# Kernel optimization log

Measured on AMD Instinct MI355X. Metric: run time of the kernel, lower is better.

## Reference

```python
import jax, jax.numpy as jnp
import numpy as np

N_NODES = 100000
N_EDGES = 1600000
NODE_DIM = 128
EDGE_DIM = 32
HIDDEN_DIM = 256


def _linear_params(key, fan_in, fan_out):
    kw, kb = jax.random.split(key)
    bound = 1.0 / np.sqrt(fan_in)
    W = jax.random.uniform(kw, (fan_in, fan_out), minval=-bound, maxval=bound, dtype=jnp.float32)
    b = jax.random.uniform(kb, (fan_out,), minval=-bound, maxval=bound, dtype=jnp.float32)
    return W, b


def setup_inputs() -> dict:
    key = jax.random.key(0)
    ks = jax.random.split(key, 8)
    x = jax.random.normal(ks[0], (N_NODES, NODE_DIM), dtype=jnp.float32)
    edge_index = jax.random.randint(ks[1], (2, N_EDGES), 0, N_NODES, dtype=jnp.int64)
    edge_attr = jax.random.normal(ks[2], (N_EDGES, EDGE_DIM), dtype=jnp.float32)
    congestion = jax.random.uniform(ks[3], (N_NODES,), dtype=jnp.float32)
    msg_in = 2 * NODE_DIM + EDGE_DIM + 1
    mW1, mb1 = _linear_params(ks[4], msg_in, HIDDEN_DIM)
    mW2, mb2 = _linear_params(ks[5], HIDDEN_DIM, NODE_DIM)
    uW1, ub1 = _linear_params(ks[6], 2 * NODE_DIM, HIDDEN_DIM)
    uW2, ub2 = _linear_params(ks[7], HIDDEN_DIM, NODE_DIM)
    return {
        "x": x, "edge_index": edge_index, "edge_attr": edge_attr, "congestion": congestion,
        "mW1": mW1, "mb1": mb1, "mW2": mW2, "mb2": mb2,
        "uW1": uW1, "ub1": ub1, "uW2": uW2, "ub2": ub2,
    }


def reference(x, edge_index, edge_attr, congestion, mW1, mb1, mW2, mb2, uW1, ub1, uW2, ub2):
    src, dst = edge_index[0], edge_index[1]
    # gather node features and src congestion, concat along feature dim  [E, 2D+edge_dim+1]
    msg_in = jnp.concatenate(
        [x[src], x[dst], edge_attr, congestion[src][:, None]], axis=-1)
    h = jax.nn.relu(msg_in @ mW1 + mb1)          # [E, hidden]
    messages = h @ mW2 + mb2                     # [E, node_dim]
    # scatter_add messages into destination nodes  [N, node_dim]
    aggregated = jax.ops.segment_sum(messages, dst, num_segments=x.shape[0])
    upd_in = jnp.concatenate([x, aggregated], axis=-1)  # [N, 2*node_dim]
    h2 = jax.nn.relu(upd_in @ uW1 + ub1)
    x_new = h2 @ uW2 + ub2                       # [N, node_dim]
    return x_new
```

## Files before the change

### kernel.cpp

```cpp
#include <hip/hip_runtime.h>

#define E_TOTAL 1600000
#define NN 100000
#define D 128
#define ED 32
#define H 256

typedef __attribute__((ext_vector_type(8))) short s16x8;
typedef __attribute__((ext_vector_type(4))) short s16x4;
typedef __attribute__((ext_vector_type(4))) float f32x4;

#define MFMA(a, b, c) __builtin_amdgcn_mfma_f32_16x16x32_bf16((a), (b), (c), 0, 0, 0)

__device__ __forceinline__ short f2bf(float f) {
    unsigned u = __builtin_bit_cast(unsigned, f);
    u += 0x7fffu + ((u >> 16) & 1u);
    return (short)(u >> 16);
}

__device__ __forceinline__ void gll16(const void* g, void* l) {
    __builtin_amdgcn_global_load_lds(
        (const __attribute__((address_space(1))) void*)g,
        (__attribute__((address_space(3))) void*)l, 16, 0, 0);
}

__global__ void k_cvt_x(const float* __restrict__ x, short* __restrict__ xb, int n) {
    int i = (blockIdx.x * blockDim.x + threadIdx.x) * 4;
    if (i >= n) return;
    f32x4 v = *(const f32x4*)(x + i);
    s16x4 o;
    o[0] = f2bf(v[0]); o[1] = f2bf(v[1]); o[2] = f2bf(v[2]); o[3] = f2bf(v[3]);
    *(s16x4*)(xb + i) = o;
}

__global__ void k_swz(const float* __restrict__ W, short* __restrict__ out,
                      int K, int N, int total) {
    int idx = blockIdx.x * blockDim.x + threadIdx.x;
    if (idx >= total) return;
    int j    = idx & 7;
    int lane = (idx >> 3) & 63;
    int rest = idx >> 9;
    int NT   = N >> 4;
    int nt   = rest % NT;
    int t    = rest / NT;
    int k    = t * 32 + (lane >> 4) * 8 + j;
    int col  = nt * 16 + (lane & 15);
    float v  = (k < K) ? W[k * N + col] : 0.f;
    out[idx] = f2bf(v);
}

__global__ void k_hist(const int* __restrict__ ei, int* __restrict__ cnt) {
    int e = blockIdx.x * blockDim.x + threadIdx.x;
    if (e >= E_TOTAL) return;
    atomicAdd(&cnt[ei[E_TOTAL + e]], 1);
}

__global__ void k_scan1(int* __restrict__ cnt, int* __restrict__ psum, int n) {
    __shared__ int wsum[16];
    __shared__ int woff[16];
    const int tid = threadIdx.x, lane = tid & 63, wv = tid >> 6;
    int i = blockIdx.x * 1024 + tid;
    int v = (i < n) ? cnt[i] : 0;
    int s = v;
#pragma unroll
    for (int off = 1; off < 64; off <<= 1) {
        int u = __shfl_up(s, off, 64);
        if (lane >= off) s += u;
    }
    if (lane == 63) wsum[wv] = s;
    __syncthreads();
    if (wv == 0 && lane < 16) {
        int t = wsum[lane];
        int sc = t;
#pragma unroll
        for (int off = 1; off < 16; off <<= 1) {
            int u = __shfl_up(sc, off, 16);
            if (lane >= off) sc += u;
        }
        woff[lane] = sc - t;
    }
    __syncthreads();
    int excl = (s - v) + woff[wv];
    if (i < n) cnt[i] = excl;
    if (tid == 1023) psum[blockIdx.x] = excl + v;
}

__global__ void k_scan2(int* __restrict__ psum, int nb) {
    __shared__ int w0;
    const int tid = threadIdx.x, lane = tid & 63, wv = tid >> 6;
    int v = (tid < nb) ? psum[tid] : 0;
    int s = v;
#pragma unroll
    for (int off = 1; off < 64; off <<= 1) {
        int u = __shfl_up(s, off, 64);
        if (lane >= off) s += u;
    }
    if (wv == 0 && lane == 63) w0 = s;
    __syncthreads();
    int excl = (s - v) + (wv ? w0 : 0);
    if (tid < nb) psum[tid] = excl;
}

__global__ void k_scan3(const int* __restrict__ psum, int* __restrict__ cnt, int n) {
    int i = blockIdx.x * 1024 + threadIdx.x;
    if (i < n) cnt[i] += psum[blockIdx.x];
}

__global__ void k_perm(const int* __restrict__ ei, int* __restrict__ cursor,
                       int* __restrict__ perm, int2* __restrict__ srcdst) {
    int e = blockIdx.x * blockDim.x + threadIdx.x;
    if (e >= E_TOTAL) return;
    int s = ei[e], d = ei[E_TOTAL + e];
    int pos = atomicAdd(&cursor[d], 1);
    perm[pos] = e;
    srcdst[pos] = make_int2(s, d);
}

__global__ __launch_bounds__(256, 2)
void k_edge(const short* __restrict__ xb, const int* __restrict__ perm,
            const int2* __restrict__ srcdst,
            const float* __restrict__ eattr, const float* __restrict__ cong,
            const short* __restrict__ W1s, const float* __restrict__ b1,
            const short* __restrict__ W2s, const float* __restrict__ b2,
            float* __restrict__ agg) {
    __shared__ char smem[73728];
    __shared__ int   dst_s[128];
    __shared__ short cong_s[128];

    const int tid  = threadIdx.x;
    const int lane = tid & 63;
    const int w    = tid >> 6;
    const int m    = lane & 15;
    const int q    = lane >> 4;
    const int p0b  = blockIdx.x * 128;

    {
        const int kqs = (lane & 3) ^ ((lane >> 4) & 3);
#pragma unroll
        for (int j = 0; j < 2; j++) {
            int el  = w * 32 + j * 16 + (lane >> 2);
            int2 sd = srcdst[p0b + el];
            int  ea = perm[p0b + el];
            char* dst = smem + (w * 2 + j) * 1024;
            const char* gx0 = (const char*)xb + (long)sd.x * 256 + kqs * 16;
            const char* gx1 = (const char*)xb + (long)sd.y * 256 + kqs * 16;
#pragma unroll
            for (int t = 0; t < 4; t++)
                gll16(gx0 + t * 64, dst + t * 8192);
#pragma unroll
            for (int t = 0; t < 4; t++)
                gll16(gx1 + t * 64, dst + (4 + t) * 8192);
            const float* ge = eattr + (long)ea * ED + kqs * 8;
            f32x4 e0 = *(const f32x4*)ge, e1 = *(const f32x4*)(ge + 4);
            s16x8 ev;
#pragma unroll
            for (int jj = 0; jj < 4; jj++) { ev[jj] = f2bf(e0[jj]); ev[4 + jj] = f2bf(e1[jj]); }
            *(s16x8*)(dst + 8 * 8192 + lane * 16) = ev;
        }
        if (tid < 128) {
            int2 sd2 = srcdst[p0b + tid];
            dst_s[tid]  = sd2.y;
            cong_s[tid] = f2bf(cong[sd2.x]);
        }
    }
    __syncthreads();

    const int rdoff = m * 64 + ((q ^ ((m >> 2) & 3)) << 4);

    f32x4 acc[8][4];
#pragma unroll
    for (int mt = 0; mt < 8; mt++)
#pragma unroll
        for (int n = 0; n < 4; n++) acc[mt][n] = (f32x4){0.f, 0.f, 0.f, 0.f};

#pragma unroll
    for (int t = 0; t < 9; t++) {
        s16x8 b[4];
        const short* bw = W1s + (t * 16 + w * 4) * 512 + lane * 8;
#pragma unroll
        for (int n = 0; n < 4; n++) b[n] = *(const s16x8*)(bw + n * 512);
#pragma unroll
        for (int mt = 0; mt < 8; mt++) {
            s16x8 a = *(const s16x8*)(smem + t * 8192 + mt * 1024 + rdoff);
#pragma unroll
            for (int n = 0; n < 4; n++) acc[mt][n] = MFMA(a, b[n], acc[mt][n]);
        }
    }
    {
        s16x8 b[4];
        const short* bw = W1s + (9 * 16 + w * 4) * 512 + lane * 8;
#pragma unroll
        for (int n = 0; n < 4; n++) b[n] = *(const s16x8*)(bw + n * 512);
#pragma unroll
        for (int mt = 0; mt < 8; mt++) {
            s16x8 a = (s16x8){0, 0, 0, 0, 0, 0, 0, 0};
            short cv = cong_s[mt * 16 + m];
            a[0] = (q == 0) ? cv : (short)0;
#pragma unroll
            for (int n = 0; n < 4; n++) acc[mt][n] = MFMA(a, b[n], acc[mt][n]);
        }
    }
    __syncthreads();

    {
        short* hb = (short*)smem;
#pragma unroll
        for (int n = 0; n < 4; n++) {
            const int chunk = 2 * w + (n >> 1);
            const int srq   = (n & 1) * 2 + (m >> 3);
            const int phys  = srq ^ q;
            const float bias = b1[w * 64 + n * 16 + m];
            const int base = chunk * 4096 + (q * 4) * 32 + phys * 8 + (m & 7);
#pragma unroll
            for (int mt = 0; mt < 8; mt++) {
#pragma unroll
                for (int r = 0; r < 4; r++) {
                    float v = acc[mt][n][r] + bias;
                    hb[base + mt * 512 + r * 32] = f2bf(v > 0.f ? v : 0.f);
                }
            }
        }
    }
    __syncthreads();

    f32x4 acc2[8][2];
#pragma unroll
    for (int mt = 0; mt < 8; mt++) {
        acc2[mt][0] = (f32x4){0.f, 0.f, 0.f, 0.f};
        acc2[mt][1] = (f32x4){0.f, 0.f, 0.f, 0.f};
    }
#pragma unroll
    for (int t2 = 0; t2 < 8; t2++) {
        s16x8 b0  = *(const s16x8*)(W2s + (t2 * 8 + w * 2) * 512 + lane * 8);
        s16x8 b1v = *(const s16x8*)(W2s + (t2 * 8 + w * 2 + 1) * 512 + lane * 8);
#pragma unroll
        for (int mt = 0; mt < 8; mt++) {
            s16x8 a = *(const s16x8*)(smem + t2 * 8192 + mt * 1024 + rdoff);
            acc2[mt][0] = MFMA(a, b0, acc2[mt][0]);
            acc2[mt][1] = MFMA(a, b1v, acc2[mt][1]);
        }
    }
    __syncthreads();

    {
        float (*mbuf)[132] = (float (*)[132])smem;
        float bb0 = b2[w * 32 + m];
        float bb1 = b2[w * 32 + 16 + m];
#pragma unroll
        for (int mt = 0; mt < 8; mt++)
#pragma unroll
            for (int r = 0; r < 4; r++) {
                mbuf[mt * 16 + q * 4 + r][w * 32 + m]      = acc2[mt][0][r] + bb0;
                mbuf[mt * 16 + q * 4 + r][w * 32 + 16 + m] = acc2[mt][1][r] + bb1;
            }
    }
    __syncthreads();

    {
        float (*mbuf)[132] = (float (*)[132])smem;
        const int half = tid >> 7, cc = tid & 127;
        float s = 0.f;
        int prev = dst_s[half * 64];
        for (int row = half * 64; row < half * 64 + 64; row++) {
            int dcur = dst_s[row];
            if (dcur != prev) {
                __hip_atomic_fetch_add(agg + (long)prev * D + cc, s,
                                       __ATOMIC_RELAXED, __HIP_MEMORY_SCOPE_AGENT);
                s = 0.f; prev = dcur;
            }
            s += mbuf[row][cc];
        }
        __hip_atomic_fetch_add(agg + (long)prev * D + cc, s,
                               __ATOMIC_RELAXED, __HIP_MEMORY_SCOPE_AGENT);
    }
}

__global__ __launch_bounds__(256, 2)
void k_node(const short* __restrict__ xb, const float* __restrict__ agg,
            const short* __restrict__ U1s, const float* __restrict__ b1,
            const short* __restrict__ U2s, const float* __restrict__ b2,
            float* __restrict__ out) {
    __shared__ char smem[65536];
    const int tid  = threadIdx.x;
    const int lane = tid & 63;
    const int w    = tid >> 6;
    const int m    = lane & 15;
    const int q    = lane >> 4;
    const int r0   = blockIdx.x * 128;

    {
        const int kqs = (lane & 3) ^ ((lane >> 4) & 3);
#pragma unroll
        for (int j = 0; j < 2; j++) {
            int rowl = w * 32 + j * 16 + (lane >> 2);
            int grow = r0 + rowl;
            int gc   = grow < NN ? grow : 0;
            char* dst = smem + (w * 2 + j) * 1024;
            const char* gx = (const char*)xb + (long)gc * 256 + kqs * 16;
#pragma unroll
            for (int t = 0; t < 4; t++)
                gll16(gx + t * 64, dst + t * 8192);
            const float* ga = agg + (long)gc * D + kqs * 8;
#pragma unroll
            for (int t = 0; t < 4; t++) {
                f32x4 a0 = *(const f32x4*)(ga + t * 32);
                f32x4 a1 = *(const f32x4*)(ga + t * 32 + 4);
                s16x8 v;
#pragma unroll
                for (int jj = 0; jj < 4; jj++) { v[jj] = f2bf(a0[jj]); v[4 + jj] = f2bf(a1[jj]); }
                *(s16x8*)(dst + (4 + t) * 8192 + lane * 16) = v;
            }
        }
    }
    __syncthreads();

    const int rdoff = m * 64 + ((q ^ ((m >> 2) & 3)) << 4);

    f32x4 acc[8][4];
#pragma unroll
    for (int mt = 0; mt < 8; mt++)
#pragma unroll
        for (int n = 0; n < 4; n++) acc[mt][n] = (f32x4){0.f, 0.f, 0.f, 0.f};

#pragma unroll
    for (int t = 0; t < 8; t++) {
        s16x8 b[4];
        const short* bw = U1s + (t * 16 + w * 4) * 512 + lane * 8;
#pragma unroll
        for (int n = 0; n < 4; n++) b[n] = *(const s16x8*)(bw + n * 512);
#pragma unroll
        for (int mt = 0; mt < 8; mt++) {
            s16x8 a = *(const s16x8*)(smem + t * 8192 + mt * 1024 + rdoff);
#pragma unroll
            for (int n = 0; n < 4; n++) acc[mt][n] = MFMA(a, b[n], acc[mt][n]);
        }
    }
    __syncthreads();

    {
        short* hb = (short*)smem;
#pragma unroll
        for (int n = 0; n < 4; n++) {
            const int chunk = 2 * w + (n >> 1);
            const int srq   = (n & 1) * 2 + (m >> 3);
            const int phys  = srq ^ q;
            const float bias = b1[w * 64 + n * 16 + m];
            const int base = chunk * 4096 + (q * 4) * 32 + phys * 8 + (m & 7);
#pragma unroll
            for (int mt = 0; mt < 8; mt++) {
#pragma unroll
                for (int r = 0; r < 4; r++) {
                    float v = acc[mt][n][r] + bias;
                    hb[base + mt * 512 + r * 32] = f2bf(v > 0.f ? v : 0.f);
                }
            }
        }
    }
    __syncthreads();

    f32x4 acc2[8][2];
#pragma unroll
    for (int mt = 0; mt < 8; mt++) {
        acc2[mt][0] = (f32x4){0.f, 0.f, 0.f, 0.f};
        acc2[mt][1] = (f32x4){0.f, 0.f, 0.f, 0.f};
    }
#pragma unroll
    for (int t2 = 0; t2 < 8; t2++) {
        s16x8 b0  = *(const s16x8*)(U2s + (t2 * 8 + w * 2) * 512 + lane * 8);
        s16x8 b1v = *(const s16x8*)(U2s + (t2 * 8 + w * 2 + 1) * 512 + lane * 8);
#pragma unroll
        for (int mt = 0; mt < 8; mt++) {
            s16x8 a = *(const s16x8*)(smem + t2 * 8192 + mt * 1024 + rdoff);
            acc2[mt][0] = MFMA(a, b0, acc2[mt][0]);
            acc2[mt][1] = MFMA(a, b1v, acc2[mt][1]);
        }
    }

    {
        float bb0 = b2[w * 32 + m];
        float bb1 = b2[w * 32 + 16 + m];
#pragma unroll
        for (int mt = 0; mt < 8; mt++)
#pragma unroll
            for (int r = 0; r < 4; r++) {
                int grow = r0 + mt * 16 + q * 4 + r;
                if (grow < NN) {
                    out[(long)grow * D + w * 32 + m]      = acc2[mt][0][r] + bb0;
                    out[(long)grow * D + w * 32 + 16 + m] = acc2[mt][1][r] + bb1;
                }
            }
    }
}

extern "C" void kernel_launch(void* const* d_in, const int* in_sizes, int n_in,
                              void* d_out, int out_size, void* d_ws, size_t ws_size,
                              hipStream_t stream) {
    const float* x     = (const float*)d_in[0];
    const int*   ei    = (const int*)d_in[1];
    const float* eattr = (const float*)d_in[2];
    const float* cong  = (const float*)d_in[3];
    const float* mW1   = (const float*)d_in[4];
    const float* mb1   = (const float*)d_in[5];
    const float* mW2   = (const float*)d_in[6];
    const float* mb2   = (const float*)d_in[7];
    const float* uW1   = (const float*)d_in[8];
    const float* ub1   = (const float*)d_in[9];
    const float* uW2   = (const float*)d_in[10];
    const float* ub2   = (const float*)d_in[11];

    char* ws = (char*)d_ws;
    float* agg    = (float*)ws;
    short* xb     = (short*)(ws + 51200000);
    short* W1s    = (short*)(ws + 76800000);
    short* W2s    = (short*)(ws + 76963840);
    short* U1s    = (short*)(ws + 77029376);
    short* U2s    = (short*)(ws + 77160448);
    int*   cnt    = (int*)(ws + 77225984);
    int*   perm   = (int*)(ws + 77625984);
    int2*  srcdst = (int2*)(ws + 84025984);
    int*   psum   = (int*)(ws + 96825984);

    hipMemsetAsync(agg, 0, (size_t)NN * D * sizeof(float), stream);
    hipMemsetAsync(cnt, 0, (size_t)NN * sizeof(int), stream);

    k_cvt_x<<<(NN * D / 4 + 255) / 256, 256, 0, stream>>>(x, xb, NN * D);

    int tW1 = 10 * 16 * 512, tW2 = 8 * 8 * 512, tU1 = 8 * 16 * 512, tU2 = 8 * 8 * 512;
    k_swz<<<(tW1 + 255) / 256, 256, 0, stream>>>(mW1, W1s, 289, 256, tW1);
    k_swz<<<(tW2 + 255) / 256, 256, 0, stream>>>(mW2, W2s, 256, 128, tW2);
    k_swz<<<(tU1 + 255) / 256, 256, 0, stream>>>(uW1, U1s, 256, 256, tU1);
    k_swz<<<(tU2 + 255) / 256, 256, 0, stream>>>(uW2, U2s, 256, 128, tU2);

    int nb = (NN + 1023) / 1024;
    k_hist<<<(E_TOTAL + 255) / 256, 256, 0, stream>>>(ei, cnt);
    k_scan1<<<nb, 1024, 0, stream>>>(cnt, psum, NN);
    k_scan2<<<1, 128, 0, stream>>>(psum, nb);
    k_scan3<<<nb, 1024, 0, stream>>>(psum, cnt, NN);
    k_perm<<<(E_TOTAL + 255) / 256, 256, 0, stream>>>(ei, cnt, perm, srcdst);

    k_edge<<<E_TOTAL / 128, 256, 0, stream>>>(xb, perm, srcdst, eattr, cong,
                                              W1s, mb1, W2s, mb2, agg);
    k_node<<<(NN + 127) / 128, 256, 0, stream>>>(xb, agg, U1s, ub1, U2s, ub2,
                                                 (float*)d_out);
}
```

Before: 1.055 ms.

## Split edge and node MLP tiles across eight waves to double occupancy

Both k_edge and k_node move from 256 to 512 threads per block. The eight waves are arranged as two row halves by four column groups, so each wave now holds a 4x4 accumulator tile instead of 8x4. The LDS staging layout and swizzle keys are reworked to match the new row ownership, and the segmented atomic reduction now runs over four 32-row quarters. The aim is to cut per-wave register pressure and fit more waves per CU to hide gather latency. In exchange, each weight fragment is loaded twice per block and the edge kernel may issue slightly more atomics.

```diff
diff --git a/kernel.cpp b/kernel.cpp
--- a/kernel.cpp
+++ b/kernel.cpp
@@ -116,7 +116,7 @@
     srcdst[pos] = make_int2(s, d);
 }
 
-__global__ __launch_bounds__(256, 2)
+__global__ __launch_bounds__(512, 4)
 void k_edge(const short* __restrict__ xb, const int* __restrict__ perm,
             const int2* __restrict__ srcdst,
             const float* __restrict__ eattr, const float* __restrict__ cong,
@@ -130,33 +130,31 @@
     const int tid  = threadIdx.x;
     const int lane = tid & 63;
     const int w    = tid >> 6;
+    const int eh   = w >> 2;
+    const int cg   = w & 3;
     const int m    = lane & 15;
     const int q    = lane >> 4;
     const int p0b  = blockIdx.x * 128;
 
     {
-        const int kqs = (lane & 3) ^ ((lane >> 4) & 3);
-#pragma unroll
-        for (int j = 0; j < 2; j++) {
-            int el  = w * 32 + j * 16 + (lane >> 2);
-            int2 sd = srcdst[p0b + el];
-            int  ea = perm[p0b + el];
-            char* dst = smem + (w * 2 + j) * 1024;
-            const char* gx0 = (const char*)xb + (long)sd.x * 256 + kqs * 16;
-            const char* gx1 = (const char*)xb + (long)sd.y * 256 + kqs * 16;
-#pragma unroll
-            for (int t = 0; t < 4; t++)
-                gll16(gx0 + t * 64, dst + t * 8192);
-#pragma unroll
-            for (int t = 0; t < 4; t++)
-                gll16(gx1 + t * 64, dst + (4 + t) * 8192);
-            const float* ge = eattr + (long)ea * ED + kqs * 8;
-            f32x4 e0 = *(const f32x4*)ge, e1 = *(const f32x4*)(ge + 4);
-            s16x8 ev;
-#pragma unroll
-            for (int jj = 0; jj < 4; jj++) { ev[jj] = f2bf(e0[jj]); ev[4 + jj] = f2bf(e1[jj]); }
-            *(s16x8*)(dst + 8 * 8192 + lane * 16) = ev;
-        }
+        int edge = w * 16 + (lane >> 2);
+        int2 sd  = srcdst[p0b + edge];
+        int kqs  = (lane & 3) ^ ((lane >> 3) & 3);
+        const char* gx0 = (const char*)xb + (long)sd.x * 256 + kqs * 16;
+        const char* gx1 = (const char*)xb + (long)sd.y * 256 + kqs * 16;
+#pragma unroll
+        for (int t = 0; t < 4; t++)
+            gll16(gx0 + t * 64, smem + t * 8192 + w * 1024);
+#pragma unroll
+        for (int t = 0; t < 4; t++)
+            gll16(gx1 + t * 64, smem + (4 + t) * 8192 + w * 1024);
+        int ea = perm[p0b + edge];
+        const float* ge = eattr + (long)ea * ED + kqs * 8;
+        f32x4 e0 = *(const f32x4*)ge, e1 = *(const f32x4*)(ge + 4);
+        s16x8 ev;
+#pragma unroll
+        for (int j = 0; j < 4; j++) { ev[j] = f2bf(e0[j]); ev[4 + j] = f2bf(e1[j]); }
+        *(s16x8*)(smem + 8 * 8192 + w * 1024 + lane * 16) = ev;
         if (tid < 128) {
             int2 sd2 = srcdst[p0b + tid];
             dst_s[tid]  = sd2.y;
@@ -165,36 +163,36 @@
     }
     __syncthreads();
 
-    const int rdoff = m * 64 + ((q ^ ((m >> 2) & 3)) << 4);
-
-    f32x4 acc[8][4];
-#pragma unroll
-    for (int mt = 0; mt < 8; mt++)
+    const int rdoff = m * 64 + ((q ^ ((m >> 1) & 3)) << 4);
+
+    f32x4 acc[4][4];
+#pragma unroll
+    for (int mt = 0; mt < 4; mt++)
 #pragma unroll
         for (int n = 0; n < 4; n++) acc[mt][n] = (f32x4){0.f, 0.f, 0.f, 0.f};
 
 #pragma unroll
     for (int t = 0; t < 9; t++) {
         s16x8 b[4];
-        const short* bw = W1s + (t * 16 + w * 4) * 512 + lane * 8;
+        const short* bw = W1s + (t * 16 + cg * 4) * 512 + lane * 8;
 #pragma unroll
         for (int n = 0; n < 4; n++) b[n] = *(const s16x8*)(bw + n * 512);
 #pragma unroll
-        for (int mt = 0; mt < 8; mt++) {
-            s16x8 a = *(const s16x8*)(smem + t * 8192 + mt * 1024 + rdoff);
+        for (int mt = 0; mt < 4; mt++) {
+            s16x8 a = *(const s16x8*)(smem + t * 8192 + (eh * 4 + mt) * 1024 + rdoff);
 #pragma unroll
             for (int n = 0; n < 4; n++) acc[mt][n] = MFMA(a, b[n], acc[mt][n]);
         }
     }
     {
         s16x8 b[4];
-        const short* bw = W1s + (9 * 16 + w * 4) * 512 + lane * 8;
+        const short* bw = W1s + (9 * 16 + cg * 4) * 512 + lane * 8;
 #pragma unroll
         for (int n = 0; n < 4; n++) b[n] = *(const s16x8*)(bw + n * 512);
 #pragma unroll
-        for (int mt = 0; mt < 8; mt++) {
+        for (int mt = 0; mt < 4; mt++) {
             s16x8 a = (s16x8){0, 0, 0, 0, 0, 0, 0, 0};
-            short cv = cong_s[mt * 16 + m];
+            short cv = cong_s[eh * 64 + mt * 16 + m];
             a[0] = (q == 0) ? cv : (short)0;
 #pragma unroll
             for (int n = 0; n < 4; n++) acc[mt][n] = MFMA(a, b[n], acc[mt][n]);
@@ -203,39 +201,42 @@
     __syncthreads();
 
     {
-        short* hb = (short*)smem;
+        short* hb16 = (short*)smem;
 #pragma unroll
         for (int n = 0; n < 4; n++) {
-            const int chunk = 2 * w + (n >> 1);
+            const int chunk = 2 * cg + (n >> 1);
             const int srq   = (n & 1) * 2 + (m >> 3);
-            const int phys  = srq ^ q;
-            const float bias = b1[w * 64 + n * 16 + m];
-            const int base = chunk * 4096 + (q * 4) * 32 + phys * 8 + (m & 7);
-#pragma unroll
-            for (int mt = 0; mt < 8; mt++) {
+            const float bias = b1[cg * 64 + n * 16 + m];
+#pragma unroll
+            for (int mt = 0; mt < 4; mt++) {
 #pragma unroll
                 for (int r = 0; r < 4; r++) {
-                    float v = acc[mt][n][r] + bias;
-                    hb[base + mt * 512 + r * 32] = f2bf(v > 0.f ? v : 0.f);
+                    int edge = eh * 64 + mt * 16 + q * 4 + r;
+                    int key  = (2 * q + (r >> 1)) & 3;
+                    int phys = srq ^ key;
+                    float v  = acc[mt][n][r] + bias;
+                    hb16[chunk * 4096 + edge * 32 + phys * 8 + (m & 7)] =
+                        f2bf(v > 0.f ? v : 0.f);
                 }
             }
         }
     }
     __syncthreads();
 
-    f32x4 acc2[8][2];
-#pragma unroll
-    for (int mt = 0; mt < 8; mt++) {
+    f32x4 acc2[4][2];
+#pragma unroll
+    for (int mt = 0; mt < 4; mt++) {
         acc2[mt][0] = (f32x4){0.f, 0.f, 0.f, 0.f};
         acc2[mt][1] = (f32x4){0.f, 0.f, 0.f, 0.f};
     }
 #pragma unroll
     for (int t2 = 0; t2 < 8; t2++) {
-        s16x8 b0  = *(const s16x8*)(W2s + (t2 * 8 + w * 2) * 512 + lane * 8);
-        s16x8 b1v = *(const s16x8*)(W2s + (t2 * 8 + w * 2 + 1) * 512 + lane * 8);
-#pragma unroll
-        for (int mt = 0; mt < 8; mt++) {
-            s16x8 a = *(const s16x8*)(smem + t2 * 8192 + mt * 1024 + rdoff);
+        const short* bw = W2s + (t2 * 8 + cg * 2) * 512 + lane * 8;
+        s16x8 b0  = *(const s16x8*)bw;
+        s16x8 b1v = *(const s16x8*)(bw + 512);
+#pragma unroll
+        for (int mt = 0; mt < 4; mt++) {
+            s16x8 a = *(const s16x8*)(smem + t2 * 8192 + (eh * 4 + mt) * 1024 + rdoff);
             acc2[mt][0] = MFMA(a, b0, acc2[mt][0]);
             acc2[mt][1] = MFMA(a, b1v, acc2[mt][1]);
         }
@@ -244,24 +245,25 @@
 
     {
         float (*mbuf)[132] = (float (*)[132])smem;
-        float bb0 = b2[w * 32 + m];
-        float bb1 = b2[w * 32 + 16 + m];
-#pragma unroll
-        for (int mt = 0; mt < 8; mt++)
+        float bb0 = b2[cg * 32 + m];
+        float bb1 = b2[cg * 32 + 16 + m];
+#pragma unroll
+        for (int mt = 0; mt < 4; mt++)
 #pragma unroll
             for (int r = 0; r < 4; r++) {
-                mbuf[mt * 16 + q * 4 + r][w * 32 + m]      = acc2[mt][0][r] + bb0;
-                mbuf[mt * 16 + q * 4 + r][w * 32 + 16 + m] = acc2[mt][1][r] + bb1;
+                int edge = eh * 64 + mt * 16 + q * 4 + r;
+                mbuf[edge][cg * 32 + m]      = acc2[mt][0][r] + bb0;
+                mbuf[edge][cg * 32 + 16 + m] = acc2[mt][1][r] + bb1;
             }
     }
     __syncthreads();
 
     {
         float (*mbuf)[132] = (float (*)[132])smem;
-        const int half = tid >> 7, cc = tid & 127;
+        const int qtr = tid >> 7, cc = tid & 127;
         float s = 0.f;
-        int prev = dst_s[half * 64];
-        for (int row = half * 64; row < half * 64 + 64; row++) {
+        int prev = dst_s[qtr * 32];
+        for (int row = qtr * 32; row < qtr * 32 + 32; row++) {
             int dcur = dst_s[row];
             if (dcur != prev) {
                 __hip_atomic_fetch_add(agg + (long)prev * D + cc, s,
@@ -275,7 +277,7 @@
     }
 }
 
-__global__ __launch_bounds__(256, 2)
+__global__ __launch_bounds__(512, 4)
 void k_node(const short* __restrict__ xb, const float* __restrict__ agg,
             const short* __restrict__ U1s, const float* __restrict__ b1,
             const short* __restrict__ U2s, const float* __restrict__ b2,
@@ -284,53 +286,51 @@
     const int tid  = threadIdx.x;
     const int lane = tid & 63;
     const int w    = tid >> 6;
+    const int eh   = w >> 2;
+    const int cg   = w & 3;
     const int m    = lane & 15;
     const int q    = lane >> 4;
     const int r0   = blockIdx.x * 128;
 
     {
-        const int kqs = (lane & 3) ^ ((lane >> 4) & 3);
-#pragma unroll
-        for (int j = 0; j < 2; j++) {
-            int rowl = w * 32 + j * 16 + (lane >> 2);
-            int grow = r0 + rowl;
-            int gc   = grow < NN ? grow : 0;
-            char* dst = smem + (w * 2 + j) * 1024;
-            const char* gx = (const char*)xb + (long)gc * 256 + kqs * 16;
-#pragma unroll
-            for (int t = 0; t < 4; t++)
-                gll16(gx + t * 64, dst + t * 8192);
-            const float* ga = agg + (long)gc * D + kqs * 8;
-#pragma unroll
-            for (int t = 0; t < 4; t++) {
-                f32x4 a0 = *(const f32x4*)(ga + t * 32);
-                f32x4 a1 = *(const f32x4*)(ga + t * 32 + 4);
-                s16x8 v;
-#pragma unroll
-                for (int jj = 0; jj < 4; jj++) { v[jj] = f2bf(a0[jj]); v[4 + jj] = f2bf(a1[jj]); }
-                *(s16x8*)(dst + (4 + t) * 8192 + lane * 16) = v;
-            }
-        }
-    }
-    __syncthreads();
-
-    const int rdoff = m * 64 + ((q ^ ((m >> 2) & 3)) << 4);
-
-    f32x4 acc[8][4];
-#pragma unroll
-    for (int mt = 0; mt < 8; mt++)
+        int rowl = w * 16 + (lane >> 2);
+        int grow = r0 + rowl;
+        int gc   = grow < NN ? grow : 0;
+        int kqs  = (lane & 3) ^ ((lane >> 3) & 3);
+        const char* gx = (const char*)xb + (long)gc * 256 + kqs * 16;
+#pragma unroll
+        for (int t = 0; t < 4; t++)
+            gll16(gx + t * 64, smem + t * 8192 + w * 1024);
+        const float* ga = agg + (long)gc * D + kqs * 8;
+#pragma unroll
+        for (int t = 0; t < 4; t++) {
+            f32x4 a0 = *(const f32x4*)(ga + t * 32);
+            f32x4 a1 = *(const f32x4*)(ga + t * 32 + 4);
+            s16x8 v;
+#pragma unroll
+            for (int j = 0; j < 4; j++) { v[j] = f2bf(a0[j]); v[4 + j] = f2bf(a1[j]); }
+            *(s16x8*)(smem + (4 + t) * 8192 + w * 1024 + lane * 16) = v;
+        }
+    }
+    __syncthreads();
+
+    const int rdoff = m * 64 + ((q ^ ((m >> 1) & 3)) << 4);
+
+    f32x4 acc[4][4];
+#pragma unroll
+    for (int mt = 0; mt < 4; mt++)
 #pragma unroll
         for (int n = 0; n < 4; n++) acc[mt][n] = (f32x4){0.f, 0.f, 0.f, 0.f};
 
 #pragma unroll
     for (int t = 0; t < 8; t++) {
         s16x8 b[4];
-        const short* bw = U1s + (t * 16 + w * 4) * 512 + lane * 8;
+        const short* bw = U1s + (t * 16 + cg * 4) * 512 + lane * 8;
 #pragma unroll
         for (int n = 0; n < 4; n++) b[n] = *(const s16x8*)(bw + n * 512);
 #pragma unroll
-        for (int mt = 0; mt < 8; mt++) {
-            s16x8 a = *(const s16x8*)(smem + t * 8192 + mt * 1024 + rdoff);
+        for (int mt = 0; mt < 4; mt++) {
+            s16x8 a = *(const s16x8*)(smem + t * 8192 + (eh * 4 + mt) * 1024 + rdoff);
 #pragma unroll
             for (int n = 0; n < 4; n++) acc[mt][n] = MFMA(a, b[n], acc[mt][n]);
         }
@@ -338,55 +338,58 @@
     __syncthreads();
 
     {
-        short* hb = (short*)smem;
+        short* hb16 = (short*)smem;
 #pragma unroll
         for (int n = 0; n < 4; n++) {
-            const int chunk = 2 * w + (n >> 1);
+            const int chunk = 2 * cg + (n >> 1);
             const int srq   = (n & 1) * 2 + (m >> 3);
-            const int phys  = srq ^ q;
-            const float bias = b1[w * 64 + n * 16 + m];
-            const int base = chunk * 4096 + (q * 4) * 32 + phys * 8 + (m & 7);
-#pragma unroll
-            for (int mt = 0; mt < 8; mt++) {
+            const float bias = b1[cg * 64 + n * 16 + m];
+#pragma unroll
+            for (int mt = 0; mt < 4; mt++) {
 #pragma unroll
                 for (int r = 0; r < 4; r++) {
+                    int row = eh * 64 + mt * 16 + q * 4 + r;
+                    int key = (2 * q + (r >> 1)) & 3;
+                    int phys = srq ^ key;
                     float v = acc[mt][n][r] + bias;
-                    hb[base + mt * 512 + r * 32] = f2bf(v > 0.f ? v : 0.f);
+                    hb16[chunk * 4096 + row * 32 + phys * 8 + (m & 7)] =
+                        f2bf(v > 0.f ? v : 0.f);
                 }
             }
         }
     }
     __syncthreads();
 
-    f32x4 acc2[8][2];
-#pragma unroll
-    for (int mt = 0; mt < 8; mt++) {
+    f32x4 acc2[4][2];
+#pragma unroll
+    for (int mt = 0; mt < 4; mt++) {
         acc2[mt][0] = (f32x4){0.f, 0.f, 0.f, 0.f};
         acc2[mt][1] = (f32x4){0.f, 0.f, 0.f, 0.f};
     }
 #pragma unroll
     for (int t2 = 0; t2 < 8; t2++) {
-        s16x8 b0  = *(const s16x8*)(U2s + (t2 * 8 + w * 2) * 512 + lane * 8);
-        s16x8 b1v = *(const s16x8*)(U2s + (t2 * 8 + w * 2 + 1) * 512 + lane * 8);
-#pragma unroll
-        for (int mt = 0; mt < 8; mt++) {
-            s16x8 a = *(const s16x8*)(smem + t2 * 8192 + mt * 1024 + rdoff);
+        const short* bw = U2s + (t2 * 8 + cg * 2) * 512 + lane * 8;
+        s16x8 b0  = *(const s16x8*)bw;
+        s16x8 b1v = *(const s16x8*)(bw + 512);
+#pragma unroll
+        for (int mt = 0; mt < 4; mt++) {
+            s16x8 a = *(const s16x8*)(smem + t2 * 8192 + (eh * 4 + mt) * 1024 + rdoff);
             acc2[mt][0] = MFMA(a, b0, acc2[mt][0]);
             acc2[mt][1] = MFMA(a, b1v, acc2[mt][1]);
         }
     }
 
     {
-        float bb0 = b2[w * 32 + m];
-        float bb1 = b2[w * 32 + 16 + m];
-#pragma unroll
-        for (int mt = 0; mt < 8; mt++)
+        float bb0 = b2[cg * 32 + m];
+        float bb1 = b2[cg * 32 + 16 + m];
+#pragma unroll
+        for (int mt = 0; mt < 4; mt++)
 #pragma unroll
             for (int r = 0; r < 4; r++) {
-                int grow = r0 + mt * 16 + q * 4 + r;
+                int grow = r0 + eh * 64 + mt * 16 + q * 4 + r;
                 if (grow < NN) {
-                    out[(long)grow * D + w * 32 + m]      = acc2[mt][0][r] + bb0;
-                    out[(long)grow * D + w * 32 + 16 + m] = acc2[mt][1][r] + bb1;
+                    out[(long)grow * D + cg * 32 + m]      = acc2[mt][0][r] + bb0;
+                    out[(long)grow * D + cg * 32 + 16 + m] = acc2[mt][1][r] + bb1;
                 }
             }
     }
@@ -438,8 +441,8 @@
     k_scan3<<<nb, 1024, 0, stream>>>(psum, cnt, NN);
     k_perm<<<(E_TOTAL + 255) / 256, 256, 0, stream>>>(ei, cnt, perm, srcdst);
 
-    k_edge<<<E_TOTAL / 128, 256, 0, stream>>>(xb, perm, srcdst, eattr, cong,
+    k_edge<<<E_TOTAL / 128, 512, 0, stream>>>(xb, perm, srcdst, eattr, cong,
                                               W1s, mb1, W2s, mb2, agg);
-    k_node<<<(NN + 127) / 128, 256, 0, stream>>>(xb, agg, U1s, ub1, U2s, ub2,
+    k_node<<<(NN + 127) / 128, 512, 0, stream>>>(xb, agg, U1s, ub1, U2s, ub2,
                                                  (float*)d_out);
 }
```

Result: faster. 935.5 us (-11.3%).
